# Optimization experiments

Hardware: AMD Instinct MI355X
Metric: run time of the kernel (lower is better)

## Reference

```python
import jax, jax.numpy as jnp
import numpy as np

N_NODES = 100000
N_EDGES = 800000


def setup_inputs() -> dict:
    key = jax.random.key(0)
    ks = jax.random.split(key, 9)
    def glorot(k, shape):
        lim = float(np.sqrt(6.0 / (shape[0] + shape[1])))
        return jax.random.uniform(k, shape, jnp.float32, -lim, lim)
    return {
        "x": jax.random.normal(ks[0], (N_NODES, 4), jnp.float32),
        "edge_index": jax.random.randint(ks[1], (2, N_EDGES), 0, N_NODES, jnp.int64),
        "edge_weight": jax.random.uniform(ks[2], (N_EDGES,), jnp.float32),
        "W1": glorot(ks[3], (4, 128)),
        "b1": jnp.zeros((128,), jnp.float32),
        "W2": glorot(ks[4], (128, 64)),
        "b2": jnp.zeros((64,), jnp.float32),
        "W3": glorot(ks[5], (64, 1)),
        "b3": jnp.zeros((1,), jnp.float32),
    }


def reference(x, edge_index, edge_weight, W1, b1, W2, b2, W3, b3):
    N = x.shape[0]
    # PyG GCNConv: add self loops (weight 1) and symmetric normalization.
    loop = jnp.arange(N)
    src = jnp.concatenate([edge_index[0], loop])  # [E+N]
    dst = jnp.concatenate([edge_index[1], loop])  # [E+N]
    w = jnp.concatenate([edge_weight, jnp.ones((N,), x.dtype)])
    deg = jax.ops.segment_sum(w, dst, num_segments=N)  # weighted in-degree
    dis = jnp.where(deg > 0, jax.lax.rsqrt(jnp.maximum(deg, 1e-12)), 0.0)
    norm = dis[src] * w * dis[dst]  # [E+N]

    def conv(h, W, b):
        h = h @ W                      # [N, F_out] transform first (F_out small)
        msg = norm[:, None] * h[src]   # gather + scale per edge
        return jax.ops.segment_sum(msg, dst, num_segments=N) + b

    h = jax.nn.relu(conv(x, W1, b1))
    h = jax.nn.relu(conv(h, W2, b2))
    return conv(h, W3, b3)
```

## Files before the change

kernel.cpp:

```cpp
#include <hip/hip_runtime.h>
#include <hip/hip_fp16.h>


constexpr int N = 100000;
constexpr int E = 800000;
constexpr int NBKT = 391;
constexpr int BCAP = 3072;
constexpr int GC = 125;
constexpr int CHUNK = 6400;

static inline int cdiv(int a, int b) { return (a + b - 1) / b; }

typedef __attribute__((ext_vector_type(8))) _Float16 f16x8;
typedef __attribute__((ext_vector_type(4))) float f32x4;

__global__ void k_zero(int* __restrict__ bucket_cursor) {
    int i = blockIdx.x * blockDim.x + threadIdx.x;
    if (i < NBKT) bucket_cursor[i] = 0;
}

__global__ __launch_bounds__(256) void k_coarse(const int* __restrict__ src,
                                                const int* __restrict__ dst,
                                                const float* __restrict__ w,
                                                int* __restrict__ bucket_cursor,
                                                int2* __restrict__ sorted) {
    __shared__ int  hist[NBKT];
    __shared__ int  lofs[512];
    __shared__ int  gbase[NBKT];
    __shared__ int2 recs[CHUNK];
    int t = threadIdx.x;
    for (int i = t; i < NBKT; i += 256) hist[i] = 0;
    __syncthreads();
    int begin = blockIdx.x * CHUNK;
    int packed[25];
#pragma unroll
    for (int i = 0; i < 25; i++) {
        int d = dst[begin + i * 256 + t];
        int b = d >> 8;
        int rank = atomicAdd(&hist[b], 1);
        packed[i] = (rank << 17) | (b << 8) | (d & 255);
    }
    __syncthreads();
    int v0 = hist[t];
    int v1 = (256 + t < NBKT) ? hist[256 + t] : 0;
    lofs[t] = v0; lofs[256 + t] = v1;
    __syncthreads();
    for (int off = 1; off < 256; off <<= 1) {
        int u0 = (t >= off) ? lofs[t - off] : 0;
        int u1 = (t >= off) ? lofs[256 + t - off] : 0;
        __syncthreads();
        lofs[t] += u0; lofs[256 + t] += u1;
        __syncthreads();
    }
    int tot0 = lofs[255];
    lofs[t] -= v0;
    lofs[256 + t] += tot0 - v1;
    __syncthreads();
    for (int i = t; i < NBKT; i += 256) {
        int h = hist[i];
        gbase[i] = h ? atomicAdd(&bucket_cursor[i], h) : 0;
    }
    __syncthreads();
#pragma unroll
    for (int i = 0; i < 25; i++) {
        int e = begin + i * 256 + t;
        int pk = packed[i];
        int b = (pk >> 8) & 511, rank = pk >> 17, dlo = pk & 255;
        recs[lofs[b] + rank] = make_int2(src[e] | (dlo << 17), __float_as_int(w[e]));
    }
    __syncthreads();
    for (int b = t; b < NBKT; b += 256) {
        int cnt = hist[b], lo = lofs[b], gb = gbase[b];
        int lim = BCAP - gb; if (cnt > lim) cnt = lim;
        int2* dstp = sorted + (size_t)b * BCAP + gb;
        for (int j = 0; j < cnt; j++) dstp[j] = recs[lo + j];
    }
}

__global__ __launch_bounds__(512) void k_fine(const int2* __restrict__ sorted,
                                              const int* __restrict__ bucket_cursor,
                                              int cap, int2* __restrict__ payload,
                                              int* __restrict__ cursor,
                                              float* __restrict__ dis) {
    __shared__ int   ncnt[256];
    __shared__ float nwsum[256];
    int t = threadIdx.x, b = blockIdx.x;
    if (t < 256) { ncnt[t] = 1; nwsum[t] = 1.0f; }
    __syncthreads();
    int cnt = bucket_cursor[b]; if (cnt > BCAP) cnt = BCAP;
    const int2* seg = sorted + (size_t)b * BCAP;
    for (int i = t; i < cnt; i += 512) {
        int2 r = seg[i];
        int s = r.x & 0x1FFFF, dlo = r.x >> 17;
        int pos = atomicAdd(&ncnt[dlo], 1);
        atomicAdd(&nwsum[dlo], __int_as_float(r.y));
        if (pos < cap)
            payload[(size_t)(b * 256 + dlo) * cap + pos] = make_int2(s, r.y);
    }
    __syncthreads();
    int n = b * 256 + t;
    if (t < 256 && n < N) {
        int c = ncnt[t]; if (c > cap) c = cap;
        int2* row = payload + (size_t)n * cap;
        row[0] = make_int2(n, __float_as_int(1.0f));
        int cpad = (c + 7) & ~7;
        for (int e = c; e < cpad; e++) row[e] = make_int2(0, 0);
        cursor[n] = c;
        dis[n] = rsqrtf(nwsum[t]);
    }
}

__global__ __launch_bounds__(256) void k_agg1(const float* __restrict__ x,
                                              const float* __restrict__ dis,
                                              const int* __restrict__ cursor,
                                              int2* __restrict__ payload, int cap,
                                              float* __restrict__ agg1) {
    int t = threadIdx.x, lane = t & 63, wave = t >> 6;
    int nsub = lane >> 4, slot = (lane >> 2) & 3, feat = lane & 3;
    int n = (blockIdx.x * 4 + wave) * 4 + nsub;
    float di = dis[n];
    int cnt = cursor[n];
    int2* row = payload + (size_t)n * cap;
    int iters = (cnt + 3) >> 2;
    float acc = 0.f;
    for (int it = 0; it < iters; it++) {
        int e = it * 4 + slot;
        int2 p = row[e];
        float nm = dis[p.x] * __int_as_float(p.y) * di;
        float xv = x[p.x * 4 + feat];
        acc = fmaf(nm, xv, acc);
        if (feat == 0) row[e].y = __float_as_int(nm);
    }
    acc += __shfl_xor(acc, 4);
    acc += __shfl_xor(acc, 8);
    if (slot == 0) agg1[n * 4 + feat] = acc;
}

constexpr int HROW = 136;
__global__ __launch_bounds__(256) void k_fused_l1(const float4* __restrict__ agg1,
                                                  const float* __restrict__ W1,
                                                  const float* __restrict__ b1,
                                                  const float* __restrict__ W2,
                                                  __half* __restrict__ y2h) {
    __shared__ _Float16 h1lds[4][16 * HROW];
    int t = threadIdx.x, wave = t >> 6, lane = t & 63;
    int q = lane >> 4, c = lane & 15;
    _Float16* sh = h1lds[wave];

    int k1 = lane, k2 = lane + 64;
    float w10 = W1[0 * 128 + k1], w11 = W1[1 * 128 + k1];
    float w12 = W1[2 * 128 + k1], w13 = W1[3 * 128 + k1], bb1 = b1[k1];
    float w20 = W1[0 * 128 + k2], w21 = W1[1 * 128 + k2];
    float w22 = W1[2 * 128 + k2], w23 = W1[3 * 128 + k2], bb2 = b1[k2];

    f16x8 Bf[4][4];
#pragma unroll
    for (int kt = 0; kt < 4; kt++)
#pragma unroll
        for (int nt = 0; nt < 4; nt++)
#pragma unroll
            for (int j = 0; j < 8; j++)
                Bf[kt][nt][j] = (_Float16)W2[(kt * 32 + q * 8 + j) * 64 + nt * 16 + c];

    int wave_id = blockIdx.x * 4 + wave;
#pragma unroll
    for (int g = 0; g < 2; g++) {
        int n0 = (wave_id * 2 + g) * 16;
        if (n0 >= N) break;
#pragma unroll
        for (int m = 0; m < 16; m++) {
            float4 a = agg1[n0 + m];
            float v1 = bb1, v2 = bb2;
            v1 = fmaf(a.x, w10, v1); v1 = fmaf(a.y, w11, v1);
            v1 = fmaf(a.z, w12, v1); v1 = fmaf(a.w, w13, v1);
            v2 = fmaf(a.x, w20, v2); v2 = fmaf(a.y, w21, v2);
            v2 = fmaf(a.z, w22, v2); v2 = fmaf(a.w, w23, v2);
            sh[m * HROW + k1] = (_Float16)fmaxf(v1, 0.f);
            sh[m * HROW + k2] = (_Float16)fmaxf(v2, 0.f);
        }
        f32x4 C[4] = {{0.f, 0.f, 0.f, 0.f}, {0.f, 0.f, 0.f, 0.f},
                      {0.f, 0.f, 0.f, 0.f}, {0.f, 0.f, 0.f, 0.f}};
#pragma unroll
        for (int kt = 0; kt < 4; kt++) {
            f16x8 A = *(const f16x8*)&sh[c * HROW + kt * 32 + q * 8];
#pragma unroll
            for (int nt = 0; nt < 4; nt++)
                C[nt] = __builtin_amdgcn_mfma_f32_16x16x32_f16(A, Bf[kt][nt], C[nt], 0, 0, 0);
        }
#pragma unroll
        for (int nt = 0; nt < 4; nt++)
#pragma unroll
            for (int r = 0; r < 4; r++) {
                int node = n0 + q * 4 + r;
                y2h[(size_t)node * 64 + nt * 16 + c] = __float2half(C[nt][r]);
            }
    }
}

__global__ __launch_bounds__(256) void k_agg2(const __half* __restrict__ y2h,
                                              const int* __restrict__ cursor,
                                              const int2* __restrict__ payload, int cap,
                                              const float* __restrict__ b2,
                                              const float* __restrict__ W3,
                                              float* __restrict__ s_out) {
    int t = threadIdx.x, lane = t & 63, wave = t >> 6;
    int nsub = lane >> 4, slot = (lane >> 3) & 1, k = lane & 7;
    int n = (blockIdx.x * 4 + wave) * 4 + nsub;
    float b2v[8], w3v[8];
#pragma unroll
    for (int j = 0; j < 8; j++) { b2v[j] = b2[k * 8 + j]; w3v[j] = W3[k * 8 + j]; }
    int cnt = cursor[n];
    const int2* row = payload + (size_t)n * cap;
    int iters = (cnt + 1) >> 1;
    float acc[8] = {0.f, 0.f, 0.f, 0.f, 0.f, 0.f, 0.f, 0.f};
    for (int it = 0; it < iters; it++) {
        int2 p = row[it * 2 + slot];
        float nm = __int_as_float(p.y);
        f16x8 v = *(const f16x8*)(y2h + (size_t)p.x * 64 + k * 8);
#pragma unroll
        for (int j = 0; j < 8; j++)
            acc[j] = fmaf(nm, (float)v[j], acc[j]);
    }
#pragma unroll
    for (int j = 0; j < 8; j++) acc[j] += __shfl_xor(acc[j], 8);
    float p_ = 0.f;
#pragma unroll
    for (int j = 0; j < 8; j++) {
        float h = fmaxf(acc[j] + b2v[j], 0.f);
        p_ = fmaf(h, w3v[j], p_);
    }
    p_ += __shfl_xor(p_, 1);
    p_ += __shfl_xor(p_, 2);
    p_ += __shfl_xor(p_, 4);
    if (slot == 0 && k == 0) s_out[n] = p_;
}

__global__ __launch_bounds__(256) void k_agg3(const float* __restrict__ s,
                                              const int* __restrict__ cursor,
                                              const int2* __restrict__ payload, int cap,
                                              const float* __restrict__ b3,
                                              float* __restrict__ out) {
    int t = threadIdx.x, lane = t & 63, wave = t >> 6;
    int nsub = lane >> 3, slot = lane & 7;
    int n = (blockIdx.x * 4 + wave) * 8 + nsub;
    int cnt = cursor[n];
    const int2* row = payload + (size_t)n * cap;
    int iters = (cnt + 7) >> 3;
    float acc = 0.f;
    for (int it = 0; it < iters; it++) {
        int2 p = row[it * 8 + slot];
        acc = fmaf(__int_as_float(p.y), s[p.x], acc);
    }
    acc += __shfl_xor(acc, 1);
    acc += __shfl_xor(acc, 2);
    acc += __shfl_xor(acc, 4);
    if (slot == 0) out[n] = acc + b3[0];
}

extern "C" void kernel_launch(void* const* d_in, const int* in_sizes, int n_in,
                              void* d_out, int out_size, void* d_ws, size_t ws_size,
                              hipStream_t stream) {
    const float* x  = (const float*)d_in[0];
    const int*   ei = (const int*)d_in[1];
    const int* src = ei;
    const int* dst = ei + E;
    const float* w  = (const float*)d_in[2];
    const float* W1 = (const float*)d_in[3];
    const float* b1 = (const float*)d_in[4];
    const float* W2 = (const float*)d_in[5];
    const float* b2 = (const float*)d_in[6];
    const float* W3 = (const float*)d_in[7];
    const float* b3 = (const float*)d_in[8];
    float* out = (float*)d_out;

    int*    bcur    = (int*)d_ws;
    int*    cursor  = bcur + 512;
    float*  dis     = (float*)(cursor + N);
    float*  agg1    = dis + N;
    __half* y2h     = (__half*)(agg1 + 4 * N);
    float*  s       = agg1;
    int2*   sorted  = (int2*)((char*)y2h + (size_t)64 * N * sizeof(__half));
    int2*   payload = sorted + (size_t)NBKT * BCAP;
    size_t fixed_bytes = (size_t)(512 + 2 * N + 4 * N) * 4 + (size_t)64 * N * 2
                       + (size_t)NBKT * BCAP * 8;
    int cap = (int)((ws_size - fixed_bytes) / ((size_t)N * 8));
    if (cap > 64) cap = 64;

    k_zero    <<<cdiv(NBKT, 256), 256, 0, stream>>>(bcur);
    k_coarse  <<<GC,              256, 0, stream>>>(src, dst, w, bcur, sorted);
    k_fine    <<<NBKT,            512, 0, stream>>>(sorted, bcur, cap, payload, cursor, dis);
    k_agg1    <<<N / 16,          256, 0, stream>>>(x, dis, cursor, payload, cap, agg1);
    k_fused_l1<<<cdiv(N / 16, 8), 256, 0, stream>>>((const float4*)agg1, W1, b1, W2, y2h);
    k_agg2    <<<N / 16,          256, 0, stream>>>(y2h, cursor, payload, cap, b2, W3, s);
    k_agg3    <<<N / 32,          256, 0, stream>>>(s, cursor, payload, cap, b3, out);
}
```

Before: 163.7 us.

## Replace atomic bucket scatter with per-block staging and fuse layer-1 aggregation

```diff
diff --git a/kernel.cpp b/kernel.cpp
--- a/kernel.cpp
+++ b/kernel.cpp
@@ -5,28 +5,23 @@
 constexpr int N = 100000;
 constexpr int E = 800000;
 constexpr int NBKT = 391;
-constexpr int BCAP = 3072;
 constexpr int GC = 125;
 constexpr int CHUNK = 6400;
+constexpr int CAP = 64;
 
 static inline int cdiv(int a, int b) { return (a + b - 1) / b; }
 
 typedef __attribute__((ext_vector_type(8))) _Float16 f16x8;
 typedef __attribute__((ext_vector_type(4))) float f32x4;
-
-__global__ void k_zero(int* __restrict__ bucket_cursor) {
-    int i = blockIdx.x * blockDim.x + threadIdx.x;
-    if (i < NBKT) bucket_cursor[i] = 0;
-}
 
 __global__ __launch_bounds__(256) void k_coarse(const int* __restrict__ src,
                                                 const int* __restrict__ dst,
                                                 const float* __restrict__ w,
-                                                int* __restrict__ bucket_cursor,
-                                                int2* __restrict__ sorted) {
+                                                int* __restrict__ cnt2d,
+                                                int* __restrict__ lofs2d,
+                                                int2* __restrict__ stage) {
     __shared__ int  hist[NBKT];
-    __shared__ int  lofs[512];
-    __shared__ int  gbase[NBKT];
+    __shared__ int  scan[512];
     __shared__ int2 recs[CHUNK];
     int t = threadIdx.x;
     for (int i = t; i < NBKT; i += 256) hist[i] = 0;
@@ -43,65 +38,78 @@
     __syncthreads();
     int v0 = hist[t];
     int v1 = (256 + t < NBKT) ? hist[256 + t] : 0;
-    lofs[t] = v0; lofs[256 + t] = v1;
+    scan[t] = v0; scan[256 + t] = v1;
     __syncthreads();
     for (int off = 1; off < 256; off <<= 1) {
-        int u0 = (t >= off) ? lofs[t - off] : 0;
-        int u1 = (t >= off) ? lofs[256 + t - off] : 0;
-        __syncthreads();
-        lofs[t] += u0; lofs[256 + t] += u1;
-        __syncthreads();
-    }
-    int tot0 = lofs[255];
-    lofs[t] -= v0;
-    lofs[256 + t] += tot0 - v1;
+        int u0 = (t >= off) ? scan[t - off] : 0;
+        int u1 = (t >= off) ? scan[256 + t - off] : 0;
+        __syncthreads();
+        scan[t] += u0; scan[256 + t] += u1;
+        __syncthreads();
+    }
+    int tot0 = scan[255];
+    scan[t] -= v0;
+    scan[256 + t] += tot0 - v1;
     __syncthreads();
     for (int i = t; i < NBKT; i += 256) {
-        int h = hist[i];
-        gbase[i] = h ? atomicAdd(&bucket_cursor[i], h) : 0;
-    }
-    __syncthreads();
+        cnt2d[blockIdx.x * NBKT + i] = hist[i];
+        lofs2d[blockIdx.x * NBKT + i] = scan[i];
+    }
 #pragma unroll
     for (int i = 0; i < 25; i++) {
         int e = begin + i * 256 + t;
         int pk = packed[i];
         int b = (pk >> 8) & 511, rank = pk >> 17, dlo = pk & 255;
-        recs[lofs[b] + rank] = make_int2(src[e] | (dlo << 17), __float_as_int(w[e]));
-    }
-    __syncthreads();
-    for (int b = t; b < NBKT; b += 256) {
-        int cnt = hist[b], lo = lofs[b], gb = gbase[b];
-        int lim = BCAP - gb; if (cnt > lim) cnt = lim;
-        int2* dstp = sorted + (size_t)b * BCAP + gb;
-        for (int j = 0; j < cnt; j++) dstp[j] = recs[lo + j];
-    }
-}
-
-__global__ __launch_bounds__(512) void k_fine(const int2* __restrict__ sorted,
-                                              const int* __restrict__ bucket_cursor,
-                                              int cap, int2* __restrict__ payload,
+        recs[scan[b] + rank] = make_int2(src[e] | (dlo << 17), __float_as_int(w[e]));
+    }
+    __syncthreads();
+    for (int i = t; i < CHUNK; i += 256)
+        stage[(size_t)blockIdx.x * CHUNK + i] = recs[i];
+}
+
+__global__ __launch_bounds__(512) void k_fine(const int* __restrict__ cnt2d,
+                                              const int* __restrict__ lofs2d,
+                                              const int2* __restrict__ stage,
+                                              int2* __restrict__ payload,
                                               int* __restrict__ cursor,
                                               float* __restrict__ dis) {
     __shared__ int   ncnt[256];
     __shared__ float nwsum[256];
+    __shared__ int   sofs[GC];
+    __shared__ int   sbase[GC + 1];
+    __shared__ int   stmp[128];
     int t = threadIdx.x, b = blockIdx.x;
     if (t < 256) { ncnt[t] = 1; nwsum[t] = 1.0f; }
-    __syncthreads();
-    int cnt = bucket_cursor[b]; if (cnt > BCAP) cnt = BCAP;
-    const int2* seg = sorted + (size_t)b * BCAP;
-    for (int i = t; i < cnt; i += 512) {
-        int2 r = seg[i];
+    int cval = 0;
+    if (t < GC) { cval = cnt2d[t * NBKT + b]; sofs[t] = lofs2d[t * NBKT + b]; }
+    if (t < 128) stmp[t] = (t < GC) ? cval : 0;
+    __syncthreads();
+    for (int off = 1; off < 128; off <<= 1) {
+        int u = (t < 128 && t >= off) ? stmp[t - off] : 0;
+        __syncthreads();
+        if (t < 128) stmp[t] += u;
+        __syncthreads();
+    }
+    if (t < GC) sbase[t] = stmp[t] - cval;
+    if (t == GC - 1) sbase[GC] = stmp[t];
+    __syncthreads();
+    int total = sbase[GC];
+    for (int i = t; i < total; i += 512) {
+        int lo = 0, hi = GC - 1;
+        while (lo < hi) { int mid = (lo + hi + 1) >> 1;
+                          if (sbase[mid] <= i) lo = mid; else hi = mid - 1; }
+        int2 r = stage[(size_t)lo * CHUNK + sofs[lo] + (i - sbase[lo])];
         int s = r.x & 0x1FFFF, dlo = r.x >> 17;
         int pos = atomicAdd(&ncnt[dlo], 1);
         atomicAdd(&nwsum[dlo], __int_as_float(r.y));
-        if (pos < cap)
-            payload[(size_t)(b * 256 + dlo) * cap + pos] = make_int2(s, r.y);
+        if (pos < CAP)
+            payload[(size_t)(b * 256 + dlo) * CAP + pos] = make_int2(s, r.y);
     }
     __syncthreads();
     int n = b * 256 + t;
     if (t < 256 && n < N) {
-        int c = ncnt[t]; if (c > cap) c = cap;
-        int2* row = payload + (size_t)n * cap;
+        int c = ncnt[t]; if (c > CAP) c = CAP;
+        int2* row = payload + (size_t)n * CAP;
         row[0] = make_int2(n, __float_as_int(1.0f));
         int cpad = (c + 7) & ~7;
         for (int e = c; e < cpad; e++) row[e] = make_int2(0, 0);
@@ -110,49 +118,48 @@
     }
 }
 
-__global__ __launch_bounds__(256) void k_agg1(const float* __restrict__ x,
-                                              const float* __restrict__ dis,
-                                              const int* __restrict__ cursor,
-                                              int2* __restrict__ payload, int cap,
-                                              float* __restrict__ agg1) {
-    int t = threadIdx.x, lane = t & 63, wave = t >> 6;
-    int nsub = lane >> 4, slot = (lane >> 2) & 3, feat = lane & 3;
-    int n = (blockIdx.x * 4 + wave) * 4 + nsub;
-    float di = dis[n];
-    int cnt = cursor[n];
-    int2* row = payload + (size_t)n * cap;
-    int iters = (cnt + 3) >> 2;
-    float acc = 0.f;
-    for (int it = 0; it < iters; it++) {
-        int e = it * 4 + slot;
-        int2 p = row[e];
-        float nm = dis[p.x] * __int_as_float(p.y) * di;
-        float xv = x[p.x * 4 + feat];
-        acc = fmaf(nm, xv, acc);
-        if (feat == 0) row[e].y = __float_as_int(nm);
-    }
-    acc += __shfl_xor(acc, 4);
-    acc += __shfl_xor(acc, 8);
-    if (slot == 0) agg1[n * 4 + feat] = acc;
-}
-
 constexpr int HROW = 136;
-__global__ __launch_bounds__(256) void k_fused_l1(const float4* __restrict__ agg1,
-                                                  const float* __restrict__ W1,
-                                                  const float* __restrict__ b1,
-                                                  const float* __restrict__ W2,
-                                                  __half* __restrict__ y2h) {
+__global__ __launch_bounds__(256) void k_l1(const float* __restrict__ x,
+                                            const float* __restrict__ dis,
+                                            const int* __restrict__ cursor,
+                                            int2* __restrict__ payload,
+                                            const float* __restrict__ W1,
+                                            const float* __restrict__ b1,
+                                            const float* __restrict__ W2,
+                                            __half* __restrict__ y2h) {
+    __shared__ float    shagg[4][64];
     __shared__ _Float16 h1lds[4][16 * HROW];
     int t = threadIdx.x, wave = t >> 6, lane = t & 63;
+    int nsub = lane >> 4, slot = (lane >> 2) & 3, feat = lane & 3;
+    int base_n = blockIdx.x * 64 + wave * 16;
+#pragma unroll
+    for (int chunk = 0; chunk < 4; chunk++) {
+        int n = base_n + chunk * 4 + nsub;
+        float acc = 0.f;
+        if (n < N) {
+            float di = dis[n];
+            int cnt = cursor[n];
+            int2* row = payload + (size_t)n * CAP;
+            int iters = (cnt + 3) >> 2;
+            for (int it = 0; it < iters; it++) {
+                int e = it * 4 + slot;
+                int2 p = row[e];
+                float nm = dis[p.x] * __int_as_float(p.y) * di;
+                acc = fmaf(nm, x[p.x * 4 + feat], acc);
+                if (feat == 0) row[e].y = __float_as_int(nm);
+            }
+        }
+        acc += __shfl_xor(acc, 4);
+        acc += __shfl_xor(acc, 8);
+        if (slot == 0) shagg[wave][(chunk * 4 + nsub) * 4 + feat] = acc;
+    }
     int q = lane >> 4, c = lane & 15;
     _Float16* sh = h1lds[wave];
-
     int k1 = lane, k2 = lane + 64;
     float w10 = W1[0 * 128 + k1], w11 = W1[1 * 128 + k1];
     float w12 = W1[2 * 128 + k1], w13 = W1[3 * 128 + k1], bb1 = b1[k1];
     float w20 = W1[0 * 128 + k2], w21 = W1[1 * 128 + k2];
     float w22 = W1[2 * 128 + k2], w23 = W1[3 * 128 + k2], bb2 = b1[k2];
-
     f16x8 Bf[4][4];
 #pragma unroll
     for (int kt = 0; kt < 4; kt++)
@@ -161,45 +168,38 @@
 #pragma unroll
             for (int j = 0; j < 8; j++)
                 Bf[kt][nt][j] = (_Float16)W2[(kt * 32 + q * 8 + j) * 64 + nt * 16 + c];
-
-    int wave_id = blockIdx.x * 4 + wave;
-#pragma unroll
-    for (int g = 0; g < 2; g++) {
-        int n0 = (wave_id * 2 + g) * 16;
-        if (n0 >= N) break;
-#pragma unroll
-        for (int m = 0; m < 16; m++) {
-            float4 a = agg1[n0 + m];
-            float v1 = bb1, v2 = bb2;
-            v1 = fmaf(a.x, w10, v1); v1 = fmaf(a.y, w11, v1);
-            v1 = fmaf(a.z, w12, v1); v1 = fmaf(a.w, w13, v1);
-            v2 = fmaf(a.x, w20, v2); v2 = fmaf(a.y, w21, v2);
-            v2 = fmaf(a.z, w22, v2); v2 = fmaf(a.w, w23, v2);
-            sh[m * HROW + k1] = (_Float16)fmaxf(v1, 0.f);
-            sh[m * HROW + k2] = (_Float16)fmaxf(v2, 0.f);
+#pragma unroll
+    for (int m = 0; m < 16; m++) {
+        float4 a = *(const float4*)&shagg[wave][m * 4];
+        float v1 = bb1, v2 = bb2;
+        v1 = fmaf(a.x, w10, v1); v1 = fmaf(a.y, w11, v1);
+        v1 = fmaf(a.z, w12, v1); v1 = fmaf(a.w, w13, v1);
+        v2 = fmaf(a.x, w20, v2); v2 = fmaf(a.y, w21, v2);
+        v2 = fmaf(a.z, w22, v2); v2 = fmaf(a.w, w23, v2);
+        sh[m * HROW + k1] = (_Float16)fmaxf(v1, 0.f);
+        sh[m * HROW + k2] = (_Float16)fmaxf(v2, 0.f);
+    }
+    f32x4 C[4] = {{0.f, 0.f, 0.f, 0.f}, {0.f, 0.f, 0.f, 0.f},
+                  {0.f, 0.f, 0.f, 0.f}, {0.f, 0.f, 0.f, 0.f}};
+#pragma unroll
+    for (int kt = 0; kt < 4; kt++) {
+        f16x8 A = *(const f16x8*)&sh[c * HROW + kt * 32 + q * 8];
+#pragma unroll
+        for (int nt = 0; nt < 4; nt++)
+            C[nt] = __builtin_amdgcn_mfma_f32_16x16x32_f16(A, Bf[kt][nt], C[nt], 0, 0, 0);
+    }
+#pragma unroll
+    for (int nt = 0; nt < 4; nt++)
+#pragma unroll
+        for (int r = 0; r < 4; r++) {
+            int node = base_n + q * 4 + r;
+            if (node < N) y2h[(size_t)node * 64 + nt * 16 + c] = __float2half(C[nt][r]);
         }
-        f32x4 C[4] = {{0.f, 0.f, 0.f, 0.f}, {0.f, 0.f, 0.f, 0.f},
-                      {0.f, 0.f, 0.f, 0.f}, {0.f, 0.f, 0.f, 0.f}};
-#pragma unroll
-        for (int kt = 0; kt < 4; kt++) {
-            f16x8 A = *(const f16x8*)&sh[c * HROW + kt * 32 + q * 8];
-#pragma unroll
-            for (int nt = 0; nt < 4; nt++)
-                C[nt] = __builtin_amdgcn_mfma_f32_16x16x32_f16(A, Bf[kt][nt], C[nt], 0, 0, 0);
-        }
-#pragma unroll
-        for (int nt = 0; nt < 4; nt++)
-#pragma unroll
-            for (int r = 0; r < 4; r++) {
-                int node = n0 + q * 4 + r;
-                y2h[(size_t)node * 64 + nt * 16 + c] = __float2half(C[nt][r]);
-            }
-    }
 }
 
 __global__ __launch_bounds__(256) void k_agg2(const __half* __restrict__ y2h,
                                               const int* __restrict__ cursor,
-                                              const int2* __restrict__ payload, int cap,
+                                              const int2* __restrict__ payload,
                                               const float* __restrict__ b2,
                                               const float* __restrict__ W3,
                                               float* __restrict__ s_out) {
@@ -210,7 +210,7 @@
 #pragma unroll
     for (int j = 0; j < 8; j++) { b2v[j] = b2[k * 8 + j]; w3v[j] = W3[k * 8 + j]; }
     int cnt = cursor[n];
-    const int2* row = payload + (size_t)n * cap;
+    const int2* row = payload + (size_t)n * CAP;
     int iters = (cnt + 1) >> 1;
     float acc[8] = {0.f, 0.f, 0.f, 0.f, 0.f, 0.f, 0.f, 0.f};
     for (int it = 0; it < iters; it++) {
@@ -237,14 +237,14 @@
 
 __global__ __launch_bounds__(256) void k_agg3(const float* __restrict__ s,
                                               const int* __restrict__ cursor,
-                                              const int2* __restrict__ payload, int cap,
+                                              const int2* __restrict__ payload,
                                               const float* __restrict__ b3,
                                               float* __restrict__ out) {
     int t = threadIdx.x, lane = t & 63, wave = t >> 6;
     int nsub = lane >> 3, slot = lane & 7;
     int n = (blockIdx.x * 4 + wave) * 8 + nsub;
     int cnt = cursor[n];
-    const int2* row = payload + (size_t)n * cap;
+    const int2* row = payload + (size_t)n * CAP;
     int iters = (cnt + 7) >> 3;
     float acc = 0.f;
     for (int it = 0; it < iters; it++) {
@@ -273,24 +273,18 @@
     const float* b3 = (const float*)d_in[8];
     float* out = (float*)d_out;
 
-    int*    bcur    = (int*)d_ws;
-    int*    cursor  = bcur + 512;
+    int*    cursor  = (int*)d_ws;
     float*  dis     = (float*)(cursor + N);
-    float*  agg1    = dis + N;
-    __half* y2h     = (__half*)(agg1 + 4 * N);
-    float*  s       = agg1;
-    int2*   sorted  = (int2*)((char*)y2h + (size_t)64 * N * sizeof(__half));
-    int2*   payload = sorted + (size_t)NBKT * BCAP;
-    size_t fixed_bytes = (size_t)(512 + 2 * N + 4 * N) * 4 + (size_t)64 * N * 2
-                       + (size_t)NBKT * BCAP * 8;
-    int cap = (int)((ws_size - fixed_bytes) / ((size_t)N * 8));
-    if (cap > 64) cap = 64;
-
-    k_zero    <<<cdiv(NBKT, 256), 256, 0, stream>>>(bcur);
-    k_coarse  <<<GC,              256, 0, stream>>>(src, dst, w, bcur, sorted);
-    k_fine    <<<NBKT,            512, 0, stream>>>(sorted, bcur, cap, payload, cursor, dis);
-    k_agg1    <<<N / 16,          256, 0, stream>>>(x, dis, cursor, payload, cap, agg1);
-    k_fused_l1<<<cdiv(N / 16, 8), 256, 0, stream>>>((const float4*)agg1, W1, b1, W2, y2h);
-    k_agg2    <<<N / 16,          256, 0, stream>>>(y2h, cursor, payload, cap, b2, W3, s);
-    k_agg3    <<<N / 32,          256, 0, stream>>>(s, cursor, payload, cap, b3, out);
-}
+    float*  s       = dis + N;
+    __half* y2h     = (__half*)(s + N);
+    int*    cnt2d   = (int*)((char*)y2h + (size_t)64 * N * sizeof(__half));
+    int*    lofs2d  = cnt2d + GC * NBKT;
+    int2*   stage   = (int2*)(lofs2d + GC * NBKT);
+    int2*   payload = stage + (size_t)GC * CHUNK;
+
+    k_coarse<<<GC,           256, 0, stream>>>(src, dst, w, cnt2d, lofs2d, stage);
+    k_fine  <<<NBKT,         512, 0, stream>>>(cnt2d, lofs2d, stage, payload, cursor, dis);
+    k_l1    <<<cdiv(N, 64),  256, 0, stream>>>(x, dis, cursor, payload, W1, b1, W2, y2h);
+    k_agg2  <<<N / 16,       256, 0, stream>>>(y2h, cursor, payload, b2, W3, s);
+    k_agg3  <<<N / 32,       256, 0, stream>>>(s, cursor, payload, b3, out);
+}
```

New measurement: 169.7 us. 1.04x slower.
